# Kernel tuning notes

Hardware: AMD Instinct MI355X
Metric: run time of the kernel (lower is better)

Reference implementation:

```python
import jax, jax.numpy as jnp
import numpy as np

N, E, G = 100000, 1600000, 2000
D_IN, D_H, D_MLP, D_OUT = 768, 128, 32, 2


def setup_inputs() -> dict:
    key = jax.random.key(0)
    ks = jax.random.split(key, 12)
    x = jax.random.normal(ks[0], (N, D_IN), dtype=jnp.float32)
    edge_index = jax.random.randint(ks[1], (2, E), 0, N, dtype=jnp.int64)
    edge_attr = jax.random.uniform(ks[2], (E, 1), dtype=jnp.float32)
    batch = jnp.sort(jax.random.randint(ks[3], (N,), 0, G, dtype=jnp.int64))
    s1 = 1.0 / np.sqrt(D_IN)
    s2 = 1.0 / np.sqrt(D_H)
    s3 = 1.0 / np.sqrt(D_MLP)
    return {
        "x": x, "edge_index": edge_index, "edge_attr": edge_attr,
        "batch": batch, "num_graphs": G,
        "W1i": jax.random.normal(ks[4], (D_IN, D_H), dtype=jnp.float32) * s1,
        "W1r": jax.random.normal(ks[5], (D_IN, D_H), dtype=jnp.float32) * s1,
        "b1": jnp.zeros((D_H,), dtype=jnp.float32),
        "W2i": jax.random.normal(ks[6], (D_H, D_H), dtype=jnp.float32) * s2,
        "W2r": jax.random.normal(ks[7], (D_H, D_H), dtype=jnp.float32) * s2,
        "b2": jnp.zeros((D_H,), dtype=jnp.float32),
        "Wl1": jax.random.normal(ks[8], (D_H, D_MLP), dtype=jnp.float32) * s2,
        "bl1": jnp.zeros((D_MLP,), dtype=jnp.float32),
        "Wl2": jax.random.normal(ks[9], (D_MLP, D_OUT), dtype=jnp.float32) * s3,
        "bl2": jnp.zeros((D_OUT,), dtype=jnp.float32),
    }


def _arma_conv(x, row, col, ew, Wi, Wr, b, n_nodes):
    # gcn_norm without self-loops: D^{-1/2} A D^{-1/2}
    deg = jax.ops.segment_sum(ew, col, num_segments=n_nodes)
    dinv = jnp.where(deg > 0, jax.lax.rsqrt(jnp.where(deg > 0, deg, 1.0)), 0.0)
    norm = dinv[row] * ew * dinv[col]
    h = x @ Wi                                   # [N, F_out]
    msg = h[row] * norm[:, None]                 # gather + scale  [E, F_out]
    agg = jax.ops.segment_sum(msg, col, num_segments=n_nodes)
    return jax.nn.relu(agg + x @ Wr + b)         # ARMA: K=1, T=1, act=ReLU


def reference(x, edge_index, edge_attr, batch, num_graphs,
              W1i, W1r, b1, W2i, W2r, b2, Wl1, bl1, Wl2, bl2):
    row, col = edge_index[0], edge_index[1]
    ew = edge_attr.reshape(-1)
    n = x.shape[0]
    h = jax.nn.elu(_arma_conv(x, row, col, ew, W1i, W1r, b1, n))
    node_x = _arma_conv(h, row, col, ew, W2i, W2r, b2, n)
    # global mean pool over graphs
    sums = jax.ops.segment_sum(node_x, batch, num_segments=num_graphs)
    cnt = jax.ops.segment_sum(jnp.ones((n,), node_x.dtype), batch, num_segments=num_graphs)
    graph_x = sums / jnp.maximum(cnt, 1.0)[:, None]
    pred = jax.nn.elu(graph_x @ Wl1 + bl1) @ Wl2 + bl2
    return pred
```

## Files before the change

kernel.cpp:

```cpp
#include <hip/hip_runtime.h>
#include <hip/hip_bf16.h>
#include <math.h>

typedef __attribute__((ext_vector_type(8))) short short8;
typedef __attribute__((ext_vector_type(4))) float f32x4;
typedef __attribute__((address_space(1))) const void gvoid;
typedef __attribute__((address_space(3))) void lvoid;

#define NC 8

__device__ __forceinline__ unsigned short f2bf(float f) {
    unsigned int u = __builtin_bit_cast(unsigned int, f);
    return (unsigned short)((u + 0x7fffu + ((u >> 16) & 1u)) >> 16);
}
__device__ __forceinline__ float b2f(short s) {
    return __builtin_bit_cast(float, ((unsigned int)(unsigned short)s) << 16);
}
__device__ __forceinline__ unsigned int cvtpk(float lo, float hi) {
    unsigned int r;
    asm("v_cvt_pk_bf16_f32 %0, %1, %2" : "=v"(r) : "v"(lo), "v"(hi));
    return r;
}

__global__ __launch_bounds__(256) void deg_hist_kernel(
    const int* __restrict__ ei, const float* __restrict__ ea,
    unsigned long long* __restrict__ packed, int* __restrict__ rank, int N, int E)
{
    int e = blockIdx.x * 256 + threadIdx.x;
    if (e >= E) return;
    const int copy = blockIdx.x & (NC - 1);
    int c = ei[(size_t)E + e];
    unsigned long long fx = (unsigned long long)(ea[e] * 1048576.0f + 0.5f);
    unsigned long long old = atomicAdd(&packed[(size_t)copy * N + c], (1ULL << 42) | fx);
    rank[e] = (int)(old >> 42);
}

__global__ __launch_bounds__(256) void scan1p_kernel(
    const unsigned long long* __restrict__ packed, int* __restrict__ out,
    int* __restrict__ blksum, int n)
{
    __shared__ int part[256];
    const int t = threadIdx.x;
    const int base = blockIdx.x * 1024 + t * 4;
    int v[4];
#pragma unroll
    for (int q = 0; q < 4; ++q) {
        int s = 0;
        if (base + q < n) {
#pragma unroll
            for (int p = 0; p < NC; ++p)
                s += (int)(packed[(size_t)p * n + base + q] >> 42);
        }
        v[q] = s;
    }
    const int s = v[0] + v[1] + v[2] + v[3];
    part[t] = s;
    __syncthreads();
    for (int off = 1; off < 256; off <<= 1) {
        int x = (t >= off) ? part[t - off] : 0;
        __syncthreads();
        part[t] += x;
        __syncthreads();
    }
    if (t == 255) blksum[blockIdx.x] = part[255];
    int run = part[t] - s;
#pragma unroll
    for (int q = 0; q < 4; ++q) {
        if (base + q < n) out[base + q] = run;
        run += v[q];
    }
}

__global__ __launch_bounds__(256) void scan1_kernel(
    const int* __restrict__ in, int* __restrict__ out, int* __restrict__ blksum, int n)
{
    __shared__ int part[256];
    const int t = threadIdx.x;
    const int base = blockIdx.x * 1024 + t * 4;
    int v[4];
#pragma unroll
    for (int q = 0; q < 4; ++q) v[q] = (base + q < n) ? in[base + q] : 0;
    const int s = v[0] + v[1] + v[2] + v[3];
    part[t] = s;
    __syncthreads();
    for (int off = 1; off < 256; off <<= 1) {
        int x = (t >= off) ? part[t - off] : 0;
        __syncthreads();
        part[t] += x;
        __syncthreads();
    }
    if (t == 255) blksum[blockIdx.x] = part[255];
    int run = part[t] - s;
#pragma unroll
    for (int q = 0; q < 4; ++q) {
        if (base + q < n) out[base + q] = run;
        run += v[q];
    }
}

__global__ __launch_bounds__(256) void scan3_kernel(
    int* __restrict__ rowptr, const int* __restrict__ blkoff,
    int* __restrict__ wpb, const unsigned long long* __restrict__ packed,
    float* __restrict__ dinv, int n, int Etot)
{
    int i = blockIdx.x * 256 + threadIdx.x;
    if (i == 0) rowptr[n] = Etot;
    if (i >= n) return;
    int base = rowptr[i] + blkoff[i >> 10];
    rowptr[i] = base;
    unsigned long long degfx = 0;
    int acc = base;
#pragma unroll
    for (int p = 0; p < NC; ++p) {
        unsigned long long v = packed[(size_t)p * n + i];
        wpb[(size_t)p * n + i] = acc;
        acc += (int)(v >> 42);
        degfx += v & ((1ULL << 42) - 1);
    }
    dinv[i] = (degfx > 0) ? rsqrtf((float)degfx * 9.5367431640625e-7f) : 0.f;
}

__global__ __launch_bounds__(256) void place_kernel(
    const int* __restrict__ ei, const float* __restrict__ ea,
    const float* __restrict__ dinv, const int* __restrict__ wpb,
    const int* __restrict__ rank, int2* __restrict__ csr, int N, int E)
{
    int e = blockIdx.x * 256 + threadIdx.x;
    if (e >= E) return;
    const int copy = blockIdx.x & (NC - 1);
    int r = ei[e];
    int c = ei[(size_t)E + e];
    float nm = dinv[r] * ea[e] * dinv[c];
    int pos = wpb[(size_t)copy * N + c] + rank[e];
    int2 rec;
    rec.x = r;
    rec.y = __builtin_bit_cast(int, nm);
    csr[pos] = rec;
}

__global__ __launch_bounds__(256) void conv_weights(
    const float* __restrict__ W1i, const float* __restrict__ W1r,
    const float* __restrict__ W2i, const float* __restrict__ W2r,
    unsigned short* __restrict__ W1t, unsigned short* __restrict__ W2t)
{
    int id = blockIdx.x * 256 + threadIdx.x;
    if (id < 256 * 768) {
        int n = id / 768, j = id % 768;
        int k = (j & ~63) | ((((j >> 3) & 7) ^ (n & 7)) << 3) | (j & 7);
        float v = (n < 128) ? W1i[k * 128 + n] : W1r[k * 128 + (n - 128)];
        W1t[id] = f2bf(v);
    } else {
        int id2 = id - 256 * 768;
        if (id2 < 128 * 256) {
            int n = id2 >> 8, j = id2 & 255;
            int k = (j & ~63) | ((((j >> 3) & 7) ^ (n & 7)) << 3) | (j & 7);
            float v = (k < 128) ? W2i[k * 128 + n] : W2r[(k - 128) * 128 + n];
            W2t[id2] = f2bf(v);
        }
    }
}

__global__ __launch_bounds__(512) void gemm_mfma_dual(
    const float* __restrict__ A, const unsigned short* __restrict__ Wt,
    const float* __restrict__ bias, unsigned short* __restrict__ outP,
    unsigned short* __restrict__ outR, int M, int K)
{
    __shared__ __align__(16) unsigned char As[2][64 * 128];
    __shared__ __align__(16) unsigned char Bs[2][256 * 128];

    const int t = threadIdx.x;
    const int m0 = blockIdx.x * 64;
    const int lane = t & 63;
    const int wid = t >> 6;
    const int wm = wid >> 2;
    const int wn = wid & 3;
    const int lr = lane & 15;
    const int lk = (lane >> 4) * 8;

    f32x4 acc[2][4] = {};

    const int sr = t >> 3;
    const int sk = (t & 7) * 8;
    const int aRow = m0 + sr;
    const bool aOk = (aRow < M);
    const float* aSrc = A + (size_t)(aOk ? aRow : 0) * K + sk;
    const int aDst = sr * 128 + ((sk * 2) ^ ((sr & 7) << 4));
    const unsigned short* bSrc = Wt + (size_t)(lane >> 3) * K + (lane & 7) * 8;

#pragma unroll
    for (int i = 0; i < 4; ++i) {
        const int chunk = i * 8 + wid;
        __builtin_amdgcn_global_load_lds(
            (gvoid*)(bSrc + (size_t)chunk * 8 * K),
            (lvoid*)(&Bs[0][chunk * 1024]), 16, 0, 0);
    }
    {
        float4 f0 = {}, f1 = {};
        if (aOk) { f0 = *(const float4*)(aSrc); f1 = *(const float4*)(aSrc + 4); }
        uint4 uv = {cvtpk(f0.x, f0.y), cvtpk(f0.z, f0.w),
                    cvtpk(f1.x, f1.y), cvtpk(f1.z, f1.w)};
        *(uint4*)(&As[0][aDst]) = uv;
    }

    for (int k0 = 0; k0 < K; k0 += 64) {
        const int cur = (k0 >> 6) & 1;
        const int nxt = cur ^ 1;
        const bool hasNext = (k0 + 64 < K);
        __syncthreads();

        float4 g0 = {}, g1 = {};
        if (hasNext) {
#pragma unroll
            for (int i = 0; i < 4; ++i) {
                const int chunk = i * 8 + wid;
                __builtin_amdgcn_global_load_lds(
                    (gvoid*)(bSrc + (size_t)chunk * 8 * K + k0 + 64),
                    (lvoid*)(&Bs[nxt][chunk * 1024]), 16, 0, 0);
            }
            if (aOk) {
                g0 = *(const float4*)(aSrc + k0 + 64);
                g1 = *(const float4*)(aSrc + k0 + 64 + 4);
            }
        }

#pragma unroll
        for (int ks = 0; ks < 2; ++ks) {
            short8 a[2], b[4];
#pragma unroll
            for (int mf = 0; mf < 2; ++mf) {
                const int r = wm * 32 + mf * 16 + lr;
                a[mf] = *(const short8*)(&As[cur][r * 128 + (((ks * 32 + lk) * 2) ^ ((r & 7) << 4))]);
            }
#pragma unroll
            for (int nf = 0; nf < 4; ++nf) {
                const int n = wn * 64 + nf * 16 + lr;
                b[nf] = *(const short8*)(&Bs[cur][n * 128 + (((ks * 32 + lk) * 2) ^ ((n & 7) << 4))]);
            }
#pragma unroll
            for (int mf = 0; mf < 2; ++mf)
#pragma unroll
                for (int nf = 0; nf < 4; ++nf)
                    acc[mf][nf] = __builtin_amdgcn_mfma_f32_16x16x32_bf16(
                        a[mf], b[nf], acc[mf][nf], 0, 0, 0);
        }

        if (hasNext) {
            uint4 uv = {cvtpk(g0.x, g0.y), cvtpk(g0.z, g0.w),
                        cvtpk(g1.x, g1.y), cvtpk(g1.z, g1.w)};
            *(uint4*)(&As[nxt][aDst]) = uv;
        }
    }

#pragma unroll
    for (int mf = 0; mf < 2; ++mf) {
#pragma unroll
        for (int nf = 0; nf < 4; ++nf) {
            const int n = wn * 64 + nf * 16 + lr;
            const f32x4 v = acc[mf][nf];
            if (n < 128) {
#pragma unroll
                for (int j = 0; j < 4; ++j) {
                    const int m = m0 + wm * 32 + mf * 16 + (lane >> 4) * 4 + j;
                    if (m < M) outP[(size_t)m * 128 + n] = f2bf(v[j]);
                }
            } else {
                const int nl = n - 128;
                const float badd = bias[nl];
#pragma unroll
                for (int j = 0; j < 4; ++j) {
                    const int m = m0 + wm * 32 + mf * 16 + (lane >> 4) * 4 + j;
                    if (m < M) outR[(size_t)m * 128 + nl] = f2bf(v[j] + badd);
                }
            }
        }
    }
}

__global__ __launch_bounds__(512) void gemm_mfma_single(
    const unsigned short* __restrict__ Aa,
    const unsigned short* __restrict__ Ah,
    const unsigned short* __restrict__ Wt,
    const float* __restrict__ bias,
    unsigned short* __restrict__ outX, int M)
{
    __shared__ __align__(16) unsigned char As[128 * 128];
    __shared__ __align__(16) unsigned char Bs[128 * 128];

    const int t = threadIdx.x;
    const int m0 = blockIdx.x * 128;
    const int lane = t & 63;
    const int wid = t >> 6;
    const int wm = wid >> 1;
    const int wn = wid & 1;
    const int lr = lane & 15;
    const int lk = (lane >> 4) * 8;

    f32x4 acc[2][4] = {};

    const int sr = t >> 2;
    const int sk = (t & 3) * 16;
    const int aRow = m0 + sr;
    const bool aOk = (aRow < M);
    const int rowSafe = aOk ? aRow : 0;
    const int sw = (sr & 7) << 4;
    const unsigned short* bSrc = Wt + (size_t)(lane >> 3) * 256 + (lane & 7) * 8;

    for (int k0 = 0; k0 < 256; k0 += 64) {
#pragma unroll
        for (int i = 0; i < 2; ++i) {
            const int chunk = i * 8 + wid;
            __builtin_amdgcn_global_load_lds(
                (gvoid*)(bSrc + (size_t)chunk * 8 * 256 + k0),
                (lvoid*)(Bs + chunk * 1024), 16, 0, 0);
        }
        const unsigned short* src =
            (k0 < 128 ? Aa : Ah) + (size_t)rowSafe * 128 + (k0 & 127) + sk;
        const short8 v0 = *(const short8*)(src);
        const short8 v1 = *(const short8*)(src + 8);
        *(short8*)(As + sr * 128 + ((sk * 2) ^ sw)) = v0;
        *(short8*)(As + sr * 128 + ((sk * 2 + 16) ^ sw)) = v1;
        __syncthreads();
#pragma unroll
        for (int ks = 0; ks < 2; ++ks) {
            short8 a[2], b[4];
#pragma unroll
            for (int mf = 0; mf < 2; ++mf) {
                const int r = wm * 32 + mf * 16 + lr;
                a[mf] = *(const short8*)(As + r * 128 + (((ks * 32 + lk) * 2) ^ ((r & 7) << 4)));
            }
#pragma unroll
            for (int nf = 0; nf < 4; ++nf) {
                const int n = wn * 64 + nf * 16 + lr;
                b[nf] = *(const short8*)(Bs + n * 128 + (((ks * 32 + lk) * 2) ^ ((n & 7) << 4)));
            }
#pragma unroll
            for (int mf = 0; mf < 2; ++mf)
#pragma unroll
                for (int nf = 0; nf < 4; ++nf)
                    acc[mf][nf] = __builtin_amdgcn_mfma_f32_16x16x32_bf16(
                        a[mf], b[nf], acc[mf][nf], 0, 0, 0);
        }
        __syncthreads();
    }

#pragma unroll
    for (int mf = 0; mf < 2; ++mf) {
#pragma unroll
        for (int nf = 0; nf < 4; ++nf) {
            const int n = wn * 64 + nf * 16 + lr;
            const float bb = bias[n];
            const f32x4 v = acc[mf][nf];
#pragma unroll
            for (int j = 0; j < 4; ++j) {
                const int m = m0 + wm * 32 + mf * 16 + (lane >> 4) * 4 + j;
                if (m < M) outX[(size_t)m * 128 + n] = f2bf(fmaxf(v[j] + bb, 0.f));
            }
        }
    }
}

__global__ __launch_bounds__(256) void agg_bias_relu(
    const unsigned short* __restrict__ P, const unsigned short* __restrict__ Rbf,
    const int* __restrict__ rowptr, const int2* __restrict__ csr,
    unsigned short* __restrict__ hout, int N)
{
    const int i = blockIdx.x * 16 + (threadIdx.x >> 4);
    const int l = threadIdx.x & 15;
    if (i >= N) return;
    const int beg = rowptr[i];
    const int end = rowptr[i + 1];
    const int c = l * 8;

    float acc0[8] = {}, acc1[8] = {}, acc2[8] = {}, acc3[8] = {};
    int j = beg;
    for (; j + 3 < end; j += 4) {
        const int2 e0 = csr[j],     e1 = csr[j + 1];
        const int2 e2 = csr[j + 2], e3 = csr[j + 3];
        const short8 v0 = *(const short8*)(P + (size_t)e0.x * 128 + c);
        const short8 v1 = *(const short8*)(P + (size_t)e1.x * 128 + c);
        const short8 v2 = *(const short8*)(P + (size_t)e2.x * 128 + c);
        const short8 v3 = *(const short8*)(P + (size_t)e3.x * 128 + c);
        const float n0 = __builtin_bit_cast(float, e0.y);
        const float n1 = __builtin_bit_cast(float, e1.y);
        const float n2 = __builtin_bit_cast(float, e2.y);
        const float n3 = __builtin_bit_cast(float, e3.y);
#pragma unroll
        for (int q = 0; q < 8; ++q) {
            acc0[q] = fmaf(b2f(v0[q]), n0, acc0[q]);
            acc1[q] = fmaf(b2f(v1[q]), n1, acc1[q]);
            acc2[q] = fmaf(b2f(v2[q]), n2, acc2[q]);
            acc3[q] = fmaf(b2f(v3[q]), n3, acc3[q]);
        }
    }
    for (; j < end; ++j) {
        const int2 e0 = csr[j];
        const short8 v0 = *(const short8*)(P + (size_t)e0.x * 128 + c);
        const float n0 = __builtin_bit_cast(float, e0.y);
#pragma unroll
        for (int q = 0; q < 8; ++q) acc0[q] = fmaf(b2f(v0[q]), n0, acc0[q]);
    }
    const short8 rv = *(const short8*)(Rbf + (size_t)i * 128 + c);
    short8 ov;
#pragma unroll
    for (int q = 0; q < 8; ++q)
        ov[q] = (short)f2bf(fmaxf((acc0[q] + acc1[q]) + (acc2[q] + acc3[q]) + b2f(rv[q]), 0.f));
    *(short8*)(hout + (size_t)i * 128 + c) = ov;
}

__global__ __launch_bounds__(256) void agg_plain(
    const unsigned short* __restrict__ H,
    const int* __restrict__ rowptr, const int2* __restrict__ csr,
    unsigned short* __restrict__ ahout, int N)
{
    const int i = blockIdx.x * 16 + (threadIdx.x >> 4);
    const int l = threadIdx.x & 15;
    if (i >= N) return;
    const int beg = rowptr[i];
    const int end = rowptr[i + 1];
    const int c = l * 8;

    float acc0[8] = {}, acc1[8] = {}, acc2[8] = {}, acc3[8] = {};
    int j = beg;
    for (; j + 3 < end; j += 4) {
        const int2 e0 = csr[j],     e1 = csr[j + 1];
        const int2 e2 = csr[j + 2], e3 = csr[j + 3];
        const short8 v0 = *(const short8*)(H + (size_t)e0.x * 128 + c);
        const short8 v1 = *(const short8*)(H + (size_t)e1.x * 128 + c);
        const short8 v2 = *(const short8*)(H + (size_t)e2.x * 128 + c);
        const short8 v3 = *(const short8*)(H + (size_t)e3.x * 128 + c);
        const float n0 = __builtin_bit_cast(float, e0.y);
        const float n1 = __builtin_bit_cast(float, e1.y);
        const float n2 = __builtin_bit_cast(float, e2.y);
        const float n3 = __builtin_bit_cast(float, e3.y);
#pragma unroll
        for (int q = 0; q < 8; ++q) {
            acc0[q] = fmaf(b2f(v0[q]), n0, acc0[q]);
            acc1[q] = fmaf(b2f(v1[q]), n1, acc1[q]);
            acc2[q] = fmaf(b2f(v2[q]), n2, acc2[q]);
            acc3[q] = fmaf(b2f(v3[q]), n3, acc3[q]);
        }
    }
    for (; j < end; ++j) {
        const int2 e0 = csr[j];
        const short8 v0 = *(const short8*)(H + (size_t)e0.x * 128 + c);
        const float n0 = __builtin_bit_cast(float, e0.y);
#pragma unroll
        for (int q = 0; q < 8; ++q) acc0[q] = fmaf(b2f(v0[q]), n0, acc0[q]);
    }
    short8 ov;
#pragma unroll
    for (int q = 0; q < 8; ++q)
        ov[q] = (short)f2bf((acc0[q] + acc1[q]) + (acc2[q] + acc3[q]));
    *(short8*)(ahout + (size_t)i * 128 + c) = ov;
}

__global__ __launch_bounds__(256) void pool_mlp(
    const unsigned short* __restrict__ nx, const int* __restrict__ batch, int N,
    const float* __restrict__ Wl1, const float* __restrict__ bl1,
    const float* __restrict__ Wl2, const float* __restrict__ bl2,
    float* __restrict__ out)
{
    __shared__ float gxp[2][128];
    __shared__ float hid[32];
    __shared__ int rng[2];
    const int g = blockIdx.x;
    const int t = threadIdx.x;
    if (t < 2) {
        const int target = g + t;
        int lo = 0, hi = N;
        while (lo < hi) {
            int mid = (lo + hi) >> 1;
            if (batch[mid] < target) lo = mid + 1; else hi = mid;
        }
        rng[t] = lo;
    }
    __syncthreads();
    const int s = rng[0], e = rng[1];
    const int col = t & 127;
    const int half = t >> 7;
    float a0 = 0.f, a1 = 0.f, a2 = 0.f, a3 = 0.f;
    int i = s + half;
    for (; i + 6 < e; i += 8) {
        a0 += b2f((short)nx[(size_t)(i + 0) * 128 + col]);
        a1 += b2f((short)nx[(size_t)(i + 2) * 128 + col]);
        a2 += b2f((short)nx[(size_t)(i + 4) * 128 + col]);
        a3 += b2f((short)nx[(size_t)(i + 6) * 128 + col]);
    }
    for (; i < e; i += 2) a0 += b2f((short)nx[(size_t)i * 128 + col]);
    gxp[half][col] = (a0 + a1) + (a2 + a3);
    __syncthreads();
    if (t < 128) gxp[0][t] = (gxp[0][t] + gxp[1][t]) / fmaxf((float)(e - s), 1.f);
    __syncthreads();
    if (t < 32) {
        float a = bl1[t];
#pragma unroll 8
        for (int k = 0; k < 128; ++k) a = fmaf(gxp[0][k], Wl1[k * 32 + t], a);
        hid[t] = a > 0.f ? a : expm1f(a);
    }
    __syncthreads();
    if (t < 2) {
        float a = bl2[t];
#pragma unroll
        for (int k = 0; k < 32; ++k) a = fmaf(hid[k], Wl2[k * 2 + t], a);
        out[(size_t)g * 2 + t] = a;
    }
}

extern "C" void kernel_launch(void* const* d_in, const int* in_sizes, int n_in,
                              void* d_out, int out_size, void* d_ws, size_t ws_size,
                              hipStream_t stream)
{
    const float* x     = (const float*)d_in[0];
    const int*   ei    = (const int*)d_in[1];
    const float* ea    = (const float*)d_in[2];
    const int*   batch = (const int*)d_in[3];
    const float* W1i   = (const float*)d_in[5];
    const float* W1r   = (const float*)d_in[6];
    const float* b1    = (const float*)d_in[7];
    const float* W2i   = (const float*)d_in[8];
    const float* W2r   = (const float*)d_in[9];
    const float* b2    = (const float*)d_in[10];
    const float* Wl1   = (const float*)d_in[11];
    const float* bl1   = (const float*)d_in[12];
    const float* Wl2   = (const float*)d_in[13];
    const float* bl2   = (const float*)d_in[14];

    const int N = in_sizes[0] / 768;
    const int E = in_sizes[2];
    const int G = out_size / 2;

    char* ws = (char*)d_ws;
    size_t off = 0;
    auto alloc = [&](size_t bytes) -> char* {
        char* p = ws + off;
        off = (off + bytes + 255) & ~(size_t)255;
        return p;
    };
    unsigned long long* packed = (unsigned long long*)alloc((size_t)NC * N * 8);
    int*   rank    = (int*)alloc((size_t)E * 4);
    int*   wpb     = (int*)alloc((size_t)NC * N * 4);
    float* dinv    = (float*)alloc((size_t)N * 4);
    int*   rowptr  = (int*)alloc((size_t)(N + 1) * 4);
    int*   blkoff  = (int*)alloc((size_t)1056 * 4);
    int*   blkdum  = (int*)alloc((size_t)4 * 4);
    int2*  csr     = (int2*)alloc((size_t)E * 8);
    unsigned short* P1   = (unsigned short*)alloc((size_t)N * 128 * 2);
    unsigned short* R1   = (unsigned short*)alloc((size_t)N * 128 * 2);
    unsigned short* hbf  = (unsigned short*)alloc((size_t)N * 128 * 2);
    unsigned short* ahb  = (unsigned short*)alloc((size_t)N * 128 * 2);
    unsigned short* nxb  = (unsigned short*)alloc((size_t)N * 128 * 2);
    unsigned short* W1t  = (unsigned short*)alloc((size_t)256 * 768 * 2);
    unsigned short* W2t  = (unsigned short*)alloc((size_t)128 * 256 * 2);

    const int eBlocks = (E + 255) / 256;
    const int nb      = (N + 1023) / 1024;
    const int nBlocks = (N + 255) / 256;
    const int aBlocks = (N + 15) / 16;

    hipMemsetAsync(packed, 0, (size_t)NC * N * 8, stream);
    deg_hist_kernel<<<eBlocks, 256, 0, stream>>>(ei, ea, packed, rank, N, E);
    scan1p_kernel<<<nb, 256, 0, stream>>>(packed, rowptr, blkoff, N);
    scan1_kernel<<<1, 256, 0, stream>>>(blkoff, blkoff, blkdum, nb);
    scan3_kernel<<<nBlocks, 256, 0, stream>>>(rowptr, blkoff, wpb, packed, dinv, N, E);
    place_kernel<<<eBlocks, 256, 0, stream>>>(ei, ea, dinv, wpb, rank, csr, N, E);
    conv_weights<<<(256 * 768 + 128 * 256 + 255) / 256, 256, 0, stream>>>(
        W1i, W1r, W2i, W2r, W1t, W2t);

    gemm_mfma_dual<<<(N + 63) / 64, 512, 0, stream>>>(x, W1t, b1, P1, R1, N, 768);
    agg_bias_relu<<<aBlocks, 256, 0, stream>>>(P1, R1, rowptr, csr, hbf, N);

    agg_plain<<<aBlocks, 256, 0, stream>>>(hbf, rowptr, csr, ahb, N);
    gemm_mfma_single<<<(N + 127) / 128, 512, 0, stream>>>(ahb, hbf, W2t, b2, nxb, N);

    pool_mlp<<<G, 256, 0, stream>>>(nxb, batch, N, Wl1, bl1, Wl2, bl2, (float*)d_out);
}
```

Before: 430.4 us.

## Store gathered node features in FP8 for both edge aggregations

The first GEMM now writes the projected features P as FP8 (e4m3 via cvt_pk_fp8) instead of bf16, and the first aggregation also emits an FP8 copy of h that the second aggregation gathers from. This halves the bytes of the random per-edge gathers in the two aggregation kernels, which are dominated by memory traffic over 1.6M edges. The pool kernel is also restructured to read two bf16 values per 32-bit load across four row streams. The cost is reduced precision in the messages, which may push the output error closer to tolerance, plus an extra FP8 write of h.

```diff
diff --git a/kernel.cpp b/kernel.cpp
--- a/kernel.cpp
+++ b/kernel.cpp
@@ -4,6 +4,7 @@
 
 typedef __attribute__((ext_vector_type(8))) short short8;
 typedef __attribute__((ext_vector_type(4))) float f32x4;
+typedef __attribute__((ext_vector_type(2))) float f32x2;
 typedef __attribute__((address_space(1))) const void gvoid;
 typedef __attribute__((address_space(3))) void lvoid;
 
@@ -20,6 +21,18 @@
     unsigned int r;
     asm("v_cvt_pk_bf16_f32 %0, %1, %2" : "=v"(r) : "v"(lo), "v"(hi));
     return r;
+}
+__device__ __forceinline__ unsigned int pk8_lo(float a, float b, unsigned int old) {
+    return (unsigned int)__builtin_amdgcn_cvt_pk_fp8_f32(a, b, (int)old, false);
+}
+__device__ __forceinline__ unsigned int pk8_hi(float a, float b, unsigned int old) {
+    return (unsigned int)__builtin_amdgcn_cvt_pk_fp8_f32(a, b, (int)old, true);
+}
+__device__ __forceinline__ f32x2 up8_lo(unsigned int v) {
+    return __builtin_amdgcn_cvt_pk_f32_fp8((int)v, false);
+}
+__device__ __forceinline__ f32x2 up8_hi(unsigned int v) {
+    return __builtin_amdgcn_cvt_pk_f32_fp8((int)v, true);
 }
 
 __global__ __launch_bounds__(256) void deg_hist_kernel(
@@ -162,7 +175,7 @@
 
 __global__ __launch_bounds__(512) void gemm_mfma_dual(
     const float* __restrict__ A, const unsigned short* __restrict__ Wt,
-    const float* __restrict__ bias, unsigned short* __restrict__ outP,
+    const float* __restrict__ bias, unsigned char* __restrict__ outP8,
     unsigned short* __restrict__ outR, int M, int K)
 {
     __shared__ __align__(16) unsigned char As[2][64 * 128];
@@ -257,19 +270,20 @@
         for (int nf = 0; nf < 4; ++nf) {
             const int n = wn * 64 + nf * 16 + lr;
             const f32x4 v = acc[mf][nf];
+            const int mb = m0 + wm * 32 + mf * 16 + (lane >> 4) * 4;
             if (n < 128) {
-#pragma unroll
-                for (int j = 0; j < 4; ++j) {
-                    const int m = m0 + wm * 32 + mf * 16 + (lane >> 4) * 4 + j;
-                    if (m < M) outP[(size_t)m * 128 + n] = f2bf(v[j]);
-                }
+                const unsigned int u01 = pk8_lo(v[0], v[1], 0u);
+                const unsigned int u23 = pk8_lo(v[2], v[3], 0u);
+                if (mb + 0 < M) outP8[(size_t)(mb + 0) * 128 + n] = (unsigned char)(u01);
+                if (mb + 1 < M) outP8[(size_t)(mb + 1) * 128 + n] = (unsigned char)(u01 >> 8);
+                if (mb + 2 < M) outP8[(size_t)(mb + 2) * 128 + n] = (unsigned char)(u23);
+                if (mb + 3 < M) outP8[(size_t)(mb + 3) * 128 + n] = (unsigned char)(u23 >> 8);
             } else {
                 const int nl = n - 128;
                 const float badd = bias[nl];
 #pragma unroll
                 for (int j = 0; j < 4; ++j) {
-                    const int m = m0 + wm * 32 + mf * 16 + (lane >> 4) * 4 + j;
-                    if (m < M) outR[(size_t)m * 128 + nl] = f2bf(v[j] + badd);
+                    if (mb + j < M) outR[(size_t)(mb + j) * 128 + nl] = f2bf(v[j] + badd);
                 }
             }
         }
@@ -360,9 +374,9 @@
 }
 
 __global__ __launch_bounds__(256) void agg_bias_relu(
-    const unsigned short* __restrict__ P, const unsigned short* __restrict__ Rbf,
+    const unsigned char* __restrict__ P8, const unsigned short* __restrict__ Rbf,
     const int* __restrict__ rowptr, const int2* __restrict__ csr,
-    unsigned short* __restrict__ hout, int N)
+    unsigned short* __restrict__ hout, unsigned char* __restrict__ h8out, int N)
 {
     const int i = blockIdx.x * 16 + (threadIdx.x >> 4);
     const int l = threadIdx.x & 15;
@@ -376,39 +390,76 @@
     for (; j + 3 < end; j += 4) {
         const int2 e0 = csr[j],     e1 = csr[j + 1];
         const int2 e2 = csr[j + 2], e3 = csr[j + 3];
-        const short8 v0 = *(const short8*)(P + (size_t)e0.x * 128 + c);
-        const short8 v1 = *(const short8*)(P + (size_t)e1.x * 128 + c);
-        const short8 v2 = *(const short8*)(P + (size_t)e2.x * 128 + c);
-        const short8 v3 = *(const short8*)(P + (size_t)e3.x * 128 + c);
+        const uint2 u0 = *(const uint2*)(P8 + (size_t)e0.x * 128 + c);
+        const uint2 u1 = *(const uint2*)(P8 + (size_t)e1.x * 128 + c);
+        const uint2 u2 = *(const uint2*)(P8 + (size_t)e2.x * 128 + c);
+        const uint2 u3 = *(const uint2*)(P8 + (size_t)e3.x * 128 + c);
         const float n0 = __builtin_bit_cast(float, e0.y);
         const float n1 = __builtin_bit_cast(float, e1.y);
         const float n2 = __builtin_bit_cast(float, e2.y);
         const float n3 = __builtin_bit_cast(float, e3.y);
-#pragma unroll
-        for (int q = 0; q < 8; ++q) {
-            acc0[q] = fmaf(b2f(v0[q]), n0, acc0[q]);
-            acc1[q] = fmaf(b2f(v1[q]), n1, acc1[q]);
-            acc2[q] = fmaf(b2f(v2[q]), n2, acc2[q]);
-            acc3[q] = fmaf(b2f(v3[q]), n3, acc3[q]);
+        {
+            const f32x2 p0 = up8_lo(u0.x), p1 = up8_hi(u0.x);
+            const f32x2 p2 = up8_lo(u0.y), p3 = up8_hi(u0.y);
+            acc0[0] = fmaf(p0.x, n0, acc0[0]); acc0[1] = fmaf(p0.y, n0, acc0[1]);
+            acc0[2] = fmaf(p1.x, n0, acc0[2]); acc0[3] = fmaf(p1.y, n0, acc0[3]);
+            acc0[4] = fmaf(p2.x, n0, acc0[4]); acc0[5] = fmaf(p2.y, n0, acc0[5]);
+            acc0[6] = fmaf(p3.x, n0, acc0[6]); acc0[7] = fmaf(p3.y, n0, acc0[7]);
+        }
+        {
+            const f32x2 p0 = up8_lo(u1.x), p1 = up8_hi(u1.x);
+            const f32x2 p2 = up8_lo(u1.y), p3 = up8_hi(u1.y);
+            acc1[0] = fmaf(p0.x, n1, acc1[0]); acc1[1] = fmaf(p0.y, n1, acc1[1]);
+            acc1[2] = fmaf(p1.x, n1, acc1[2]); acc1[3] = fmaf(p1.y, n1, acc1[3]);
+            acc1[4] = fmaf(p2.x, n1, acc1[4]); acc1[5] = fmaf(p2.y, n1, acc1[5]);
+            acc1[6] = fmaf(p3.x, n1, acc1[6]); acc1[7] = fmaf(p3.y, n1, acc1[7]);
+        }
+        {
+            const f32x2 p0 = up8_lo(u2.x), p1 = up8_hi(u2.x);
+            const f32x2 p2 = up8_lo(u2.y), p3 = up8_hi(u2.y);
+            acc2[0] = fmaf(p0.x, n2, acc2[0]); acc2[1] = fmaf(p0.y, n2, acc2[1]);
+            acc2[2] = fmaf(p1.x, n2, acc2[2]); acc2[3] = fmaf(p1.y, n2, acc2[3]);
+            acc2[4] = fmaf(p2.x, n2, acc2[4]); acc2[5] = fmaf(p2.y, n2, acc2[5]);
+            acc2[6] = fmaf(p3.x, n2, acc2[6]); acc2[7] = fmaf(p3.y, n2, acc2[7]);
+        }
+        {
+            const f32x2 p0 = up8_lo(u3.x), p1 = up8_hi(u3.x);
+            const f32x2 p2 = up8_lo(u3.y), p3 = up8_hi(u3.y);
+            acc3[0] = fmaf(p0.x, n3, acc3[0]); acc3[1] = fmaf(p0.y, n3, acc3[1]);
+            acc3[2] = fmaf(p1.x, n3, acc3[2]); acc3[3] = fmaf(p1.y, n3, acc3[3]);
+            acc3[4] = fmaf(p2.x, n3, acc3[4]); acc3[5] = fmaf(p2.y, n3, acc3[5]);
+            acc3[6] = fmaf(p3.x, n3, acc3[6]); acc3[7] = fmaf(p3.y, n3, acc3[7]);
         }
     }
     for (; j < end; ++j) {
         const int2 e0 = csr[j];
-        const short8 v0 = *(const short8*)(P + (size_t)e0.x * 128 + c);
+        const uint2 u0 = *(const uint2*)(P8 + (size_t)e0.x * 128 + c);
         const float n0 = __builtin_bit_cast(float, e0.y);
-#pragma unroll
-        for (int q = 0; q < 8; ++q) acc0[q] = fmaf(b2f(v0[q]), n0, acc0[q]);
+        const f32x2 p0 = up8_lo(u0.x), p1 = up8_hi(u0.x);
+        const f32x2 p2 = up8_lo(u0.y), p3 = up8_hi(u0.y);
+        acc0[0] = fmaf(p0.x, n0, acc0[0]); acc0[1] = fmaf(p0.y, n0, acc0[1]);
+        acc0[2] = fmaf(p1.x, n0, acc0[2]); acc0[3] = fmaf(p1.y, n0, acc0[3]);
+        acc0[4] = fmaf(p2.x, n0, acc0[4]); acc0[5] = fmaf(p2.y, n0, acc0[5]);
+        acc0[6] = fmaf(p3.x, n0, acc0[6]); acc0[7] = fmaf(p3.y, n0, acc0[7]);
     }
     const short8 rv = *(const short8*)(Rbf + (size_t)i * 128 + c);
+    float s[8];
     short8 ov;
 #pragma unroll
-    for (int q = 0; q < 8; ++q)
-        ov[q] = (short)f2bf(fmaxf((acc0[q] + acc1[q]) + (acc2[q] + acc3[q]) + b2f(rv[q]), 0.f));
+    for (int q = 0; q < 8; ++q) {
+        s[q] = fmaxf((acc0[q] + acc1[q]) + (acc2[q] + acc3[q]) + b2f(rv[q]), 0.f);
+        ov[q] = (short)f2bf(s[q]);
+    }
     *(short8*)(hout + (size_t)i * 128 + c) = ov;
+    unsigned int w0 = 0, w1 = 0;
+    w0 = pk8_lo(s[0], s[1], w0); w0 = pk8_hi(s[2], s[3], w0);
+    w1 = pk8_lo(s[4], s[5], w1); w1 = pk8_hi(s[6], s[7], w1);
+    uint2 wv = {w0, w1};
+    *(uint2*)(h8out + (size_t)i * 128 + c) = wv;
 }
 
 __global__ __launch_bounds__(256) void agg_plain(
-    const unsigned short* __restrict__ H,
+    const unsigned char* __restrict__ H8,
     const int* __restrict__ rowptr, const int2* __restrict__ csr,
     unsigned short* __restrict__ ahout, int N)
 {
@@ -424,28 +475,57 @@
     for (; j + 3 < end; j += 4) {
         const int2 e0 = csr[j],     e1 = csr[j + 1];
         const int2 e2 = csr[j + 2], e3 = csr[j + 3];
-        const short8 v0 = *(const short8*)(H + (size_t)e0.x * 128 + c);
-        const short8 v1 = *(const short8*)(H + (size_t)e1.x * 128 + c);
-        const short8 v2 = *(const short8*)(H + (size_t)e2.x * 128 + c);
-        const short8 v3 = *(const short8*)(H + (size_t)e3.x * 128 + c);
+        const uint2 u0 = *(const uint2*)(H8 + (size_t)e0.x * 128 + c);
+        const uint2 u1 = *(const uint2*)(H8 + (size_t)e1.x * 128 + c);
+        const uint2 u2 = *(const uint2*)(H8 + (size_t)e2.x * 128 + c);
+        const uint2 u3 = *(const uint2*)(H8 + (size_t)e3.x * 128 + c);
         const float n0 = __builtin_bit_cast(float, e0.y);
         const float n1 = __builtin_bit_cast(float, e1.y);
         const float n2 = __builtin_bit_cast(float, e2.y);
         const float n3 = __builtin_bit_cast(float, e3.y);
-#pragma unroll
-        for (int q = 0; q < 8; ++q) {
-            acc0[q] = fmaf(b2f(v0[q]), n0, acc0[q]);
-            acc1[q] = fmaf(b2f(v1[q]), n1, acc1[q]);
-            acc2[q] = fmaf(b2f(v2[q]), n2, acc2[q]);
-            acc3[q] = fmaf(b2f(v3[q]), n3, acc3[q]);
+        {
+            const f32x2 p0 = up8_lo(u0.x), p1 = up8_hi(u0.x);
+            const f32x2 p2 = up8_lo(u0.y), p3 = up8_hi(u0.y);
+            acc0[0] = fmaf(p0.x, n0, acc0[0]); acc0[1] = fmaf(p0.y, n0, acc0[1]);
+            acc0[2] = fmaf(p1.x, n0, acc0[2]); acc0[3] = fmaf(p1.y, n0, acc0[3]);
+            acc0[4] = fmaf(p2.x, n0, acc0[4]); acc0[5] = fmaf(p2.y, n0, acc0[5]);
+            acc0[6] = fmaf(p3.x, n0, acc0[6]); acc0[7] = fmaf(p3.y, n0, acc0[7]);
+        }
+        {
+            const f32x2 p0 = up8_lo(u1.x), p1 = up8_hi(u1.x);
+            const f32x2 p2 = up8_lo(u1.y), p3 = up8_hi(u1.y);
+            acc1[0] = fmaf(p0.x, n1, acc1[0]); acc1[1] = fmaf(p0.y, n1, acc1[1]);
+            acc1[2] = fmaf(p1.x, n1, acc1[2]); acc1[3] = fmaf(p1.y, n1, acc1[3]);
+            acc1[4] = fmaf(p2.x, n1, acc1[4]); acc1[5] = fmaf(p2.y, n1, acc1[5]);
+            acc1[6] = fmaf(p3.x, n1, acc1[6]); acc1[7] = fmaf(p3.y, n1, acc1[7]);
+        }
+        {
+            const f32x2 p0 = up8_lo(u2.x), p1 = up8_hi(u2.x);
+            const f32x2 p2 = up8_lo(u2.y), p3 = up8_hi(u2.y);
+            acc2[0] = fmaf(p0.x, n2, acc2[0]); acc2[1] = fmaf(p0.y, n2, acc2[1]);
+            acc2[2] = fmaf(p1.x, n2, acc2[2]); acc2[3] = fmaf(p1.y, n2, acc2[3]);
+            acc2[4] = fmaf(p2.x, n2, acc2[4]); acc2[5] = fmaf(p2.y, n2, acc2[5]);
+            acc2[6] = fmaf(p3.x, n2, acc2[6]); acc2[7] = fmaf(p3.y, n2, acc2[7]);
+        }
+        {
+            const f32x2 p0 = up8_lo(u3.x), p1 = up8_hi(u3.x);
+            const f32x2 p2 = up8_lo(u3.y), p3 = up8_hi(u3.y);
+            acc3[0] = fmaf(p0.x, n3, acc3[0]); acc3[1] = fmaf(p0.y, n3, acc3[1]);
+            acc3[2] = fmaf(p1.x, n3, acc3[2]); acc3[3] = fmaf(p1.y, n3, acc3[3]);
+            acc3[4] = fmaf(p2.x, n3, acc3[4]); acc3[5] = fmaf(p2.y, n3, acc3[5]);
+            acc3[6] = fmaf(p3.x, n3, acc3[6]); acc3[7] = fmaf(p3.y, n3, acc3[7]);
         }
     }
     for (; j < end; ++j) {
         const int2 e0 = csr[j];
-        const short8 v0 = *(const short8*)(H + (size_t)e0.x * 128 + c);
+        const uint2 u0 = *(const uint2*)(H8 + (size_t)e0.x * 128 + c);
         const float n0 = __builtin_bit_cast(float, e0.y);
-#pragma unroll
-        for (int q = 0; q < 8; ++q) acc0[q] = fmaf(b2f(v0[q]), n0, acc0[q]);
+        const f32x2 p0 = up8_lo(u0.x), p1 = up8_hi(u0.x);
+        const f32x2 p2 = up8_lo(u0.y), p3 = up8_hi(u0.y);
+        acc0[0] = fmaf(p0.x, n0, acc0[0]); acc0[1] = fmaf(p0.y, n0, acc0[1]);
+        acc0[2] = fmaf(p1.x, n0, acc0[2]); acc0[3] = fmaf(p1.y, n0, acc0[3]);
+        acc0[4] = fmaf(p2.x, n0, acc0[4]); acc0[5] = fmaf(p2.y, n0, acc0[5]);
+        acc0[6] = fmaf(p3.x, n0, acc0[6]); acc0[7] = fmaf(p3.y, n0, acc0[7]);
     }
     short8 ov;
 #pragma unroll
@@ -460,7 +540,7 @@
     const float* __restrict__ Wl2, const float* __restrict__ bl2,
     float* __restrict__ out)
 {
-    __shared__ float gxp[2][128];
+    __shared__ float gxp[4][128];
     __shared__ float hid[32];
     __shared__ int rng[2];
     const int g = blockIdx.x;
@@ -476,20 +556,27 @@
     }
     __syncthreads();
     const int s = rng[0], e = rng[1];
-    const int col = t & 127;
-    const int half = t >> 7;
-    float a0 = 0.f, a1 = 0.f, a2 = 0.f, a3 = 0.f;
-    int i = s + half;
-    for (; i + 6 < e; i += 8) {
-        a0 += b2f((short)nx[(size_t)(i + 0) * 128 + col]);
-        a1 += b2f((short)nx[(size_t)(i + 2) * 128 + col]);
-        a2 += b2f((short)nx[(size_t)(i + 4) * 128 + col]);
-        a3 += b2f((short)nx[(size_t)(i + 6) * 128 + col]);
-    }
-    for (; i < e; i += 2) a0 += b2f((short)nx[(size_t)i * 128 + col]);
-    gxp[half][col] = (a0 + a1) + (a2 + a3);
+    const int pr = t & 63;
+    const int strm = t >> 6;
+    float a0 = 0.f, b0 = 0.f, a1 = 0.f, b1 = 0.f;
+    int i = s + strm;
+    for (; i + 4 < e; i += 8) {
+        const unsigned int u = *(const unsigned int*)&nx[(size_t)i * 128 + pr * 2];
+        const unsigned int v = *(const unsigned int*)&nx[(size_t)(i + 4) * 128 + pr * 2];
+        a0 += b2f((short)(u & 0xffff)); b0 += b2f((short)(u >> 16));
+        a1 += b2f((short)(v & 0xffff)); b1 += b2f((short)(v >> 16));
+    }
+    if (i < e) {
+        const unsigned int u = *(const unsigned int*)&nx[(size_t)i * 128 + pr * 2];
+        a0 += b2f((short)(u & 0xffff)); b0 += b2f((short)(u >> 16));
+    }
+    gxp[strm][pr * 2] = a0 + a1;
+    gxp[strm][pr * 2 + 1] = b0 + b1;
     __syncthreads();
-    if (t < 128) gxp[0][t] = (gxp[0][t] + gxp[1][t]) / fmaxf((float)(e - s), 1.f);
+    if (t < 128) {
+        gxp[0][t] = ((gxp[0][t] + gxp[1][t]) + (gxp[2][t] + gxp[3][t]))
+                    / fmaxf((float)(e - s), 1.f);
+    }
     __syncthreads();
     if (t < 32) {
         float a = bl1[t];
@@ -544,7 +631,8 @@
     int*   blkoff  = (int*)alloc((size_t)1056 * 4);
     int*   blkdum  = (int*)alloc((size_t)4 * 4);
     int2*  csr     = (int2*)alloc((size_t)E * 8);
-    unsigned short* P1   = (unsigned short*)alloc((size_t)N * 128 * 2);
+    unsigned char*  P8   = (unsigned char*)alloc((size_t)N * 128);
+    unsigned char*  H8   = (unsigned char*)alloc((size_t)N * 128);
     unsigned short* R1   = (unsigned short*)alloc((size_t)N * 128 * 2);
     unsigned short* hbf  = (unsigned short*)alloc((size_t)N * 128 * 2);
     unsigned short* ahb  = (unsigned short*)alloc((size_t)N * 128 * 2);
@@ -557,7 +645,7 @@
     const int nBlocks = (N + 255) / 256;
     const int aBlocks = (N + 15) / 16;
 
-    hipMemsetAsync(packed, 0, (size_t)NC * N * 8, stream);
+    (void)hipMemsetAsync(packed, 0, (size_t)NC * N * 8, stream);
     deg_hist_kernel<<<eBlocks, 256, 0, stream>>>(ei, ea, packed, rank, N, E);
     scan1p_kernel<<<nb, 256, 0, stream>>>(packed, rowptr, blkoff, N);
     scan1_kernel<<<1, 256, 0, stream>>>(blkoff, blkoff, blkdum, nb);
@@ -566,10 +654,10 @@
     conv_weights<<<(256 * 768 + 128 * 256 + 255) / 256, 256, 0, stream>>>(
         W1i, W1r, W2i, W2r, W1t, W2t);
 
-    gemm_mfma_dual<<<(N + 63) / 64, 512, 0, stream>>>(x, W1t, b1, P1, R1, N, 768);
-    agg_bias_relu<<<aBlocks, 256, 0, stream>>>(P1, R1, rowptr, csr, hbf, N);
-
-    agg_plain<<<aBlocks, 256, 0, stream>>>(hbf, rowptr, csr, ahb, N);
+    gemm_mfma_dual<<<(N + 63) / 64, 512, 0, stream>>>(x, W1t, b1, P8, R1, N, 768);
+    agg_bias_relu<<<aBlocks, 256, 0, stream>>>(P8, R1, rowptr, csr, hbf, H8, N);
+
+    agg_plain<<<aBlocks, 256, 0, stream>>>(H8, rowptr, csr, ahb, N);
     gemm_mfma_single<<<(N + 127) / 128, 512, 0, stream>>>(ahb, hbf, W2t, b2, nxb, N);
 
     pool_mlp<<<G, 256, 0, stream>>>(nxb, batch, N, Wl1, bl1, Wl2, bl2, (float*)d_out);
```

After: 380.7 us. 11.6% less time.
